# Kernel optimization log

Hardware: AMD Instinct MI355X
Metric: run time of the kernel (lower is better)

Reference implementation:

```python
import jax, jax.numpy as jnp
import numpy as np

B, L, C = 2, 2048, 256
H, HD = 8, 32          # num_heads, head_dim
BS = 16                # block_size
WS = 64                # slide_window_size
SK = 16                # select_k
SCALE = 1.0 / np.sqrt(HD)
NEG = -10000.0


def setup_inputs() -> dict:
    key = jax.random.key(0)
    ks = jax.random.split(key, 16)
    lin = lambda k, sh: jax.random.normal(k, sh, jnp.float32) * (1.0 / np.sqrt(sh[0]))
    return {
        "query": jax.random.normal(ks[0], (B, L, C), jnp.float32),
        "key": jax.random.normal(ks[1], (B, L, C), jnp.float32),
        "value": jax.random.normal(ks[2], (B, L, C), jnp.float32),
        "Wq": lin(ks[3], (C, C)), "bq": jnp.zeros((C,), jnp.float32),
        "Wk": lin(ks[4], (C, C)), "bk": jnp.zeros((C,), jnp.float32),
        "Wv": lin(ks[5], (C, C)), "bv": jnp.zeros((C,), jnp.float32),
        "Wo": lin(ks[6], (C, C)), "bo": jnp.zeros((C,), jnp.float32),
        "WKc": jax.random.normal(ks[7], (BS, 1), jnp.float32) * 0.25,
        "WVc": jax.random.normal(ks[8], (BS, 1), jnp.float32) * 0.25,
        "Wpe": jax.random.normal(ks[9], (BS, C), jnp.float32) * 0.02,
        "Wg": lin(ks[10], (C, 3)), "bg": jnp.zeros((3,), jnp.float32),
    }


def _heads(x):  # [B,T,C] -> [B,H,T,HD]
    return x.reshape(B, -1, H, HD).transpose(0, 2, 1, 3)


def _merge(x):  # [B,H,T,HD] -> [B,T,C]
    return x.transpose(0, 2, 1, 3).reshape(B, -1, C)


def _compressed(q, k, v, WKc, WVc, Wpe):
    nb = L // BS
    pe = Wpe[:, :HD]                                   # [BS,HD]
    kb = k.reshape(B, H, nb, BS, HD) + pe              # [B,H,nb,BS,HD]
    vb = v.reshape(B, H, nb, BS, HD) + pe
    Kc = jnp.einsum('bhnsd,s->bhnd', kb, WKc[:, 0])    # [B,H,nb,HD]
    Vc = jnp.einsum('bhnsd,s->bhnd', vb, WVc[:, 0])
    scores = jnp.einsum('bhqd,bhkd->bhqk', q, Kc) * SCALE
    w = jax.nn.softmax(scores, axis=-1)
    return _merge(jnp.einsum('bhqk,bhkd->bhqd', w, Vc))


def _selection(q, k, v):
    scores = jnp.einsum('bhqd,bhkd->bhqk', q, k) * SCALE   # [B,H,L,S]
    _, idx = jax.lax.top_k(scores, SK)                     # [B,H,L,SK]
    gather = lambda t: jnp.take_along_axis(t[:, :, None, :, :], idx[..., None], axis=3)
    k_sel = gather(k)                                      # [B,H,L,SK,HD]
    v_sel = gather(v)
    s = jnp.einsum('bhqd,bhqkd->bhqk', q, k_sel) * SCALE
    w = jax.nn.softmax(s, axis=-1)
    return _merge(jnp.einsum('bhqk,bhqkd->bhqd', w, v_sel))


def _window(q, k, v):
    i = jnp.arange(L)
    mask = jnp.abs(i[:, None] - i[None, :]) <= (min(WS, L) // 2)   # [L,L]
    scores = jnp.einsum('bhqd,bhkd->bhqk', q, k) * SCALE
    scores = jnp.where(mask[None, None], scores, NEG)
    w = jax.nn.softmax(scores, axis=-1)
    return _merge(jnp.einsum('bhqk,bhkd->bhqd', w, v))


def reference(query, key, value, Wq, bq, Wk, bk, Wv, bv, Wo, bo, WKc, WVc, Wpe, Wg, bg):
    q = _heads(query @ Wq + bq)
    k = _heads(key @ Wk + bk)
    v = _heads(value @ Wv + bv)
    o_cmp = _compressed(q, k, v, WKc, WVc, Wpe)
    o_slc = _selection(q, k, v)
    o_win = _window(q, k, v)
    gate = jax.nn.sigmoid(query @ Wg + bg)                 # [B,L,3]
    out = gate[:, :, 0:1] * o_cmp + gate[:, :, 1:2] * o_slc + gate[:, :, 2:3] * o_win
    return out @ Wo + bo
```

## Files before the change

kernel.cpp:

```cpp
#include <hip/hip_runtime.h>
#include <math.h>


#define Bc 2
#define Lc 2048
#define Cc 256
#define Hc 8
#define HDc 32
#define BHc 16
#define NBc 128
#define ROWSc 4096
#define TROWSc 32768
#define SCALEc 0.17677669529663687f

typedef unsigned long long u64;
typedef __attribute__((ext_vector_type(8))) short short8v;
typedef __attribute__((ext_vector_type(4))) float f32x4;


__device__ __forceinline__ float dot32q(const float* qr, const float* kr) {
  const float4* k4 = (const float4*)kr;
  float p0 = 0.f, p1 = 0.f, p2 = 0.f, p3 = 0.f;
#pragma unroll
  for (int j = 0; j < 8; j += 4) {
    float4 a = k4[j], b = k4[j + 1], c = k4[j + 2], e = k4[j + 3];
    p0 += a.x * qr[4 * j + 0] + a.y * qr[4 * j + 1] + a.z * qr[4 * j + 2] + a.w * qr[4 * j + 3];
    p1 += b.x * qr[4 * j + 4] + b.y * qr[4 * j + 5] + b.z * qr[4 * j + 6] + b.w * qr[4 * j + 7];
    p2 += c.x * qr[4 * j + 8] + c.y * qr[4 * j + 9] + c.z * qr[4 * j + 10] + c.w * qr[4 * j + 11];
    p3 += e.x * qr[4 * j + 12] + e.y * qr[4 * j + 13] + e.z * qr[4 * j + 14] + e.w * qr[4 * j + 15];
  }
  return (p0 + p1) + (p2 + p3);
}

__device__ __forceinline__ unsigned short bf16rne(float f) {
  const unsigned u = __float_as_uint(f);
  return (unsigned short)((u + 0x7fffu + ((u >> 16) & 1u)) >> 16);
}

__device__ __forceinline__ int f2o(float x) {
  const int i = __float_as_int(x);
  return i >= 0 ? i : (i ^ 0x7fffffff);
}

__global__ __launch_bounds__(256) void proj_kernel(const float* __restrict__ X,
                                                   const float* __restrict__ W,
                                                   const float* __restrict__ bias,
                                                   float* __restrict__ outp, int headlayout) {
  __shared__ float xs[8 * Cc];
  const int tid = threadIdx.x;
  const int row0 = blockIdx.x * 8;
  {
    const float4* xin = (const float4*)(X + (size_t)row0 * Cc);
    float4* xsv = (float4*)xs;
    xsv[tid] = xin[tid];
    xsv[tid + 256] = xin[tid + 256];
  }
  __syncthreads();
  const int c0 = (tid & 63) * 4;
  const int rh = tid >> 6;
  float acc[2][4];
#pragma unroll
  for (int r = 0; r < 2; ++r)
#pragma unroll
    for (int c = 0; c < 4; ++c) acc[r][c] = 0.f;

#pragma unroll 4
  for (int d4 = 0; d4 < 64; ++d4) {
    const int d = d4 * 4;
    const float4 w0 = *(const float4*)(W + (size_t)(d + 0) * Cc + c0);
    const float4 w1 = *(const float4*)(W + (size_t)(d + 1) * Cc + c0);
    const float4 w2 = *(const float4*)(W + (size_t)(d + 2) * Cc + c0);
    const float4 w3 = *(const float4*)(W + (size_t)(d + 3) * Cc + c0);
#pragma unroll
    for (int r = 0; r < 2; ++r) {
      const float4 xv = *(const float4*)(xs + (rh * 2 + r) * Cc + d);
      acc[r][0] += xv.x * w0.x + xv.y * w1.x + xv.z * w2.x + xv.w * w3.x;
      acc[r][1] += xv.x * w0.y + xv.y * w1.y + xv.z * w2.y + xv.w * w3.y;
      acc[r][2] += xv.x * w0.z + xv.y * w1.z + xv.z * w2.z + xv.w * w3.z;
      acc[r][3] += xv.x * w0.w + xv.y * w1.w + xv.z * w2.w + xv.w * w3.w;
    }
  }
  const float4 bv = *(const float4*)(bias + c0);
#pragma unroll
  for (int r = 0; r < 2; ++r) {
    const int grow = row0 + rh * 2 + r;
    const float4 o = make_float4(acc[r][0] + bv.x, acc[r][1] + bv.y,
                                 acc[r][2] + bv.z, acc[r][3] + bv.w);
    if (headlayout) {
      const int b = grow >> 11, l = grow & 2047;
      const int h = c0 >> 5, dd = c0 & 31;
      *(float4*)(outp + (((size_t)(b * Hc + h) * Lc + l) * HDc + dd)) = o;
    } else {
      *(float4*)(outp + (size_t)grow * Cc + c0) = o;
    }
  }
}

__global__ __launch_bounds__(256) void gate_kernel(const float* __restrict__ query,
                                                   const float* __restrict__ Wg,
                                                   const float* __restrict__ bg,
                                                   float* __restrict__ gatep) {
  const int row = blockIdx.x * 256 + threadIdx.x;
  const float4* x4 = (const float4*)(query + (size_t)row * Cc);
  float a0 = bg[0], a1 = bg[1], a2 = bg[2];
#pragma unroll 8
  for (int d4 = 0; d4 < 64; ++d4) {
    const float4 xv = x4[d4];
    const float* wr = Wg + d4 * 12;
    a0 += xv.x * wr[0] + xv.y * wr[3] + xv.z * wr[6] + xv.w * wr[9];
    a1 += xv.x * wr[1] + xv.y * wr[4] + xv.z * wr[7] + xv.w * wr[10];
    a2 += xv.x * wr[2] + xv.y * wr[5] + xv.z * wr[8] + xv.w * wr[11];
  }
  float* g = gatep + (size_t)row * 3;
  g[0] = 1.f / (1.f + __expf(-a0));
  g[1] = 1.f / (1.f + __expf(-a1));
  g[2] = 1.f / (1.f + __expf(-a2));
}

__global__ __launch_bounds__(256) void cmpkv_kernel(const float* __restrict__ kh,
                                                    const float* __restrict__ vh,
                                                    const float* __restrict__ WKc,
                                                    const float* __restrict__ WVc,
                                                    const float* __restrict__ Wpe,
                                                    float* __restrict__ Kcp,
                                                    float* __restrict__ Vcp) {
  const int idx = blockIdx.x * 256 + threadIdx.x;
  const int d = idx & 31, n = (idx >> 5) & 127, bh = idx >> 12;
  float pk = 0.f, pv = 0.f;
#pragma unroll
  for (int s = 0; s < 16; ++s) {
    const float pe = Wpe[s * Cc + d];
    pk += pe * WKc[s];
    pv += pe * WVc[s];
  }
  const float* kp = kh + ((size_t)bh * Lc + n * 16) * HDc + d;
  const float* vp = vh + ((size_t)bh * Lc + n * 16) * HDc + d;
  float ak = pk, av = pv;
#pragma unroll
  for (int s = 0; s < 16; ++s) {
    ak += kp[s * HDc] * WKc[s];
    av += vp[s * HDc] * WVc[s];
  }
  Kcp[idx] = ak;
  Vcp[idx] = av;
}

__global__ __launch_bounds__(512) void cmp_attn_kernel(const float* __restrict__ qh,
                                                       const float* __restrict__ Kcp,
                                                       const float* __restrict__ Vcp,
                                                       float* __restrict__ ocmp) {
  __shared__ float sc[128][65];
  __shared__ float pm[8][64];
  const int tid = threadIdx.x, lane = tid & 63;
  const int w = __builtin_amdgcn_readfirstlane(tid >> 6);
  const int bh = blockIdx.y;
  const int lrow = blockIdx.x * 64 + lane;
  const float* q = qh + ((size_t)bh * Lc + lrow) * HDc;
  float qr[HDc];
#pragma unroll
  for (int d = 0; d < HDc; ++d) qr[d] = q[d] * SCALEc;
  const float* kcb = Kcp + (size_t)bh * NBc * HDc;
  float pmax = -1e30f;
#pragma unroll
  for (int i = 0; i < 16; ++i) {
    const int key = w * 16 + i;
    const float s = dot32q(qr, kcb + (size_t)key * HDc);
    sc[key][lane] = s;
    pmax = fmaxf(pmax, s);
  }
  pm[w][lane] = pmax;
  __syncthreads();

  const int row = tid >> 3;
  const int dg = (tid & 7) * 4;
  float m = pm[0][row];
#pragma unroll
  for (int i = 1; i < 8; ++i) m = fmaxf(m, pm[i][row]);
  const float* vcb = Vcp + (size_t)bh * NBc * HDc + dg;
  float o0 = 0.f, o1 = 0.f, o2 = 0.f, o3 = 0.f, z = 0.f;
#pragma unroll 4
  for (int key = 0; key < 128; ++key) {
    const float wgt = __expf(sc[key][row] - m);
    z += wgt;
    const float4 v = *(const float4*)(vcb + key * HDc);
    o0 += wgt * v.x; o1 += wgt * v.y; o2 += wgt * v.z; o3 += wgt * v.w;
  }
  const float iz = 1.f / z;
  *(float4*)(ocmp + ((size_t)bh * Lc + blockIdx.x * 64 + row) * HDc + dg) =
      make_float4(o0 * iz, o1 * iz, o2 * iz, o3 * iz);
}

__global__ __launch_bounds__(256) void cvtbf16_kernel(const float* __restrict__ qh,
                                                      const float* __restrict__ kh,
                                                      unsigned short* __restrict__ qhb,
                                                      unsigned short* __restrict__ khb) {
  const int gid = blockIdx.x * 256 + threadIdx.x;
  const int half = (TROWSc * HDc) / 4;
  const float* src = gid < half ? qh : kh;
  unsigned short* dst = gid < half ? qhb : khb;
  const int i = (gid < half ? gid : gid - half) * 4;
  const float4 v = *(const float4*)(src + i);
  ushort4 o;
  o.x = bf16rne(v.x);
  o.y = bf16rne(v.y);
  o.z = bf16rne(v.z);
  o.w = bf16rne(v.w);
  *(ushort4*)(dst + i) = o;
}

__global__ __launch_bounds__(512) void mfma_sel_kernel(
    const unsigned short* __restrict__ qhb,
    const unsigned short* __restrict__ khb,
    const float* __restrict__ qh,
    const float* __restrict__ kh,
    const float* __restrict__ vh,
    float* __restrict__ oslc) {
  __shared__ unsigned char pnl[16][2064];
  __shared__ float candv[8][16];
  __shared__ unsigned candk[8][128];
  __shared__ u64 ords[8][128];
  const int tid = threadIdx.x, lane = tid & 63;
  const int w = __builtin_amdgcn_readfirstlane(tid >> 6);
  const int g = lane >> 4;
  const int mn = lane & 15;
  const int bh = blockIdx.y;
  const int r0 = blockIdx.x * 16;

  const short8v qa =
      *(const short8v*)(qhb + ((size_t)bh * Lc + r0 + mn) * HDc + g * 8);
#pragma unroll
  for (int it = 0; it < 2; ++it) {
    const int k0 = w * 256 + it * 128;
    const unsigned short* kbase = khb + ((size_t)bh * Lc + k0) * HDc + g * 8;
    f32x4 acc0 = {0.f, 0.f, 0.f, 0.f}, acc1 = acc0, acc2 = acc0, acc3 = acc0;
    f32x4 acc4 = acc0, acc5 = acc0, acc6 = acc0, acc7 = acc0;
#define MM(i, dstv)                                                            \
  {                                                                            \
    const short8v kb = *(const short8v*)(kbase + (size_t)((i)*16 + mn) * HDc); \
    dstv = __builtin_amdgcn_mfma_f32_16x16x32_bf16(qa, kb, dstv, 0, 0, 0);     \
  }
    MM(0, acc0) MM(1, acc1) MM(2, acc2) MM(3, acc3)
    MM(4, acc4) MM(5, acc5) MM(6, acc6) MM(7, acc7)
#undef MM
#define QSTORE(t, accv)                                                        \
  {                                                                            \
    _Pragma("unroll") for (int r = 0; r < 4; ++r) {                            \
      const float s = accv[r] * SCALEc;                                        \
      int qi = (int)(s * 16.f + 128.f);                                        \
      qi = qi < 0 ? 0 : (qi > 255 ? 255 : qi);                                 \
      pnl[4 * g + r][k0 + (t)*16 + mn] = (unsigned char)qi;                    \
    }                                                                          \
  }
    QSTORE(0, acc0) QSTORE(1, acc1) QSTORE(2, acc2) QSTORE(3, acc3)
    QSTORE(4, acc4) QSTORE(5, acc5) QSTORE(6, acc6) QSTORE(7, acc7)
#undef QSTORE
  }
  __syncthreads();

#pragma unroll 1
  for (int rr = 0; rr < 2; ++rr) {
    const int row = w * 2 + rr;
    const int l = r0 + row;
    const int r = bh * Lc + l;

    unsigned wds[8];
#pragma unroll
    for (int j = 0; j < 8; ++j)
      wds[j] = *(const unsigned*)&pnl[row][lane * 4 + j * 256];
    int q[32];
#pragma unroll
    for (int wi = 0; wi < 8; ++wi) {
      q[4 * wi + 0] = (int)(wds[wi] & 255u);
      q[4 * wi + 1] = (int)((wds[wi] >> 8) & 255u);
      q[4 * wi + 2] = (int)((wds[wi] >> 16) & 255u);
      q[4 * wi + 3] = (int)(wds[wi] >> 24);
    }
    int mq = 0;
#pragma unroll
    for (int i = 0; i < 32; ++i) mq = max(mq, q[i]);

    int T8 = 0;
#pragma unroll
    for (int b = 7; b >= 0; --b) {
      const int trial = T8 | (1 << b);
      const int c = (int)__popcll(__ballot(mq >= trial));
      if (c >= 16) T8 = trial;
    }
    const int thr = T8 - 5;

    candk[w][lane] = 0x7fffffffu;
    candk[w][64 + lane] = 0x7fffffffu;
    __asm__ volatile("s_waitcnt lgkmcnt(0)" ::: "memory");
    int base = 0;
#pragma unroll
    for (int i = 0; i < 32; ++i) {
      const bool p_ = q[i] >= thr;
      const unsigned long long bm_ = __ballot(p_);
      if (bm_) {
        if (p_) {
          const int pos_ =
              base + (int)__builtin_amdgcn_mbcnt_hi(
                         (unsigned)(bm_ >> 32),
                         __builtin_amdgcn_mbcnt_lo((unsigned)bm_, 0u));
          if (pos_ < 128)
            candk[w][pos_] = (unsigned)((i >> 2) * 256 + lane * 4 + (i & 3));
        }
        base += (int)__popcll(bm_);
      }
    }
    const int cnt = base < 128 ? base : 128;
    __asm__ volatile("s_waitcnt lgkmcnt(0)" ::: "memory");

    const float* qp = qh + (size_t)r * HDc;
    float qr[HDc];
#pragma unroll
    for (int d = 0; d < HDc; ++d) qr[d] = qp[d] * SCALEc;
    const float* kb = kh + (size_t)bh * Lc * HDc;

    const bool vA = (lane < cnt);
    const bool vB = (64 + lane < cnt);
    const unsigned kA = candk[w][lane];
    const unsigned kB = candk[w][64 + lane];
    const float sA = dot32q(qr, kb + (size_t)(vA ? kA : 0u) * HDc);
    const float sB = dot32q(qr, kb + (size_t)(vB ? kB : 0u) * HDc);
    const u64 ordA =
        vA ? (((u64)((unsigned)f2o(sA) ^ 0x80000000u) << 12) | (u64)(2047u - kA))
           : 0ull;
    const u64 ordB =
        vB ? (((u64)((unsigned)f2o(sB) ^ 0x80000000u) << 12) | (u64)(2047u - kB))
           : 0ull;

    ords[w][lane] = ordA;
    ords[w][64 + lane] = ordB;
    __asm__ volatile("s_waitcnt lgkmcnt(0)" ::: "memory");
    int rankA = 0, rankB = 0;
#pragma unroll 4
    for (int i = 0; i < cnt; ++i) {
      const u64 o = ords[w][i];
      rankA += (o > ordA) ? 1 : 0;
      rankB += (o > ordB) ? 1 : 0;
    }
    if (vA && rankA < 16) {
      candv[w][rankA] = sA;
      candk[w][rankA] = kA;
    }
    if (vB && rankB < 16) {
      candv[w][rankB] = sB;
      candk[w][rankB] = kB;
    }
    __asm__ volatile("s_waitcnt lgkmcnt(0)" ::: "memory");

    float mtop = candv[w][0];
#pragma unroll
    for (int i = 1; i < 16; ++i) mtop = fmaxf(mtop, candv[w][i]);
    const int d = lane & 31;
    const float* vb = vh + (size_t)bh * Lc * HDc + d;
    float z = 0.f, oacc = 0.f;
#pragma unroll
    for (int i = 0; i < 16; ++i) {
      const float w_ = __expf(candv[w][i] - mtop);
      z += w_;
      oacc += w_ * vb[(size_t)candk[w][i] * HDc];
    }
    if (lane < 32) oslc[((size_t)bh * Lc + l) * HDc + d] = oacc / z;
  }
}

__global__ __launch_bounds__(512) void win_attn_kernel(const float* __restrict__ qh,
                                                       const float* __restrict__ kh,
                                                       const float* __restrict__ vh,
                                                       float* __restrict__ owin) {
  __shared__ float sc[128][65];
  __shared__ float pm[8][64];
  const int tid = threadIdx.x, lane = tid & 63;
  const int w = __builtin_amdgcn_readfirstlane(tid >> 6);
  const int bh = blockIdx.y;
  const int l0 = blockIdx.x * 64;
  const int lrow = l0 + lane;
  const float* q = qh + ((size_t)bh * Lc + lrow) * HDc;
  float qr[HDc];
#pragma unroll
  for (int d = 0; d < HDc; ++d) qr[d] = q[d] * SCALEc;
  const float* kb = kh + (size_t)bh * Lc * HDc;
  float pmax = -1e30f;
#pragma unroll
  for (int i = 0; i < 16; ++i) {
    const int j = w * 16 + i;
    const int key = l0 - 32 + j;
    const int keyc = min(max(key, 0), Lc - 1);
    float s = dot32q(qr, kb + (size_t)keyc * HDc);
    const int delta = key - lrow;
    const bool ok = (key >= 0) && (key < Lc) && (delta >= -32) && (delta <= 32);
    s = ok ? s : -1e30f;
    sc[j][lane] = s;
    pmax = fmaxf(pmax, s);
  }
  pm[w][lane] = pmax;
  __syncthreads();

  const int row = tid >> 3;
  const int dg = (tid & 7) * 4;
  float m = pm[0][row];
#pragma unroll
  for (int i = 1; i < 8; ++i) m = fmaxf(m, pm[i][row]);
  const float* vb = vh + (size_t)bh * Lc * HDc + dg;
  float o0 = 0.f, o1 = 0.f, o2 = 0.f, o3 = 0.f, z = 0.f;
#pragma unroll 4
  for (int j = 0; j < 128; ++j) {
    const float wgt = __expf(sc[j][row] - m);
    z += wgt;
    const int keyc = min(max(l0 - 32 + j, 0), Lc - 1);
    const float4 v = *(const float4*)(vb + (size_t)keyc * HDc);
    o0 += wgt * v.x; o1 += wgt * v.y; o2 += wgt * v.z; o3 += wgt * v.w;
  }
  const float iz = 1.f / z;
  *(float4*)(owin + ((size_t)bh * Lc + l0 + row) * HDc + dg) =
      make_float4(o0 * iz, o1 * iz, o2 * iz, o3 * iz);
}

__global__ __launch_bounds__(256) void combine_kernel(const float* __restrict__ ocmp,
                                                      const float* __restrict__ oslc,
                                                      const float* __restrict__ owin,
                                                      const float* __restrict__ gatep,
                                                      float* __restrict__ xm) {
  const int idx = blockIdx.x * 256 + threadIdx.x;
  const int c4 = idx & 63, grow = idx >> 6;
  const int b = grow >> 11, l = grow & 2047;
  const int h = c4 >> 3, d4 = (c4 & 7) * 4;
  const size_t hoff = (((size_t)(b * Hc + h) * Lc + l)) * HDc + d4;
  const float g0 = gatep[(size_t)grow * 3 + 0];
  const float g1 = gatep[(size_t)grow * 3 + 1];
  const float g2 = gatep[(size_t)grow * 3 + 2];
  const float4 a = *(const float4*)(ocmp + hoff);
  const float4 s = *(const float4*)(oslc + hoff);
  const float4 w = *(const float4*)(owin + hoff);
  float4 r;
  r.x = g0 * a.x + g1 * s.x + g2 * w.x;
  r.y = g0 * a.y + g1 * s.y + g2 * w.y;
  r.z = g0 * a.z + g1 * s.z + g2 * w.z;
  r.w = g0 * a.w + g1 * s.w + g2 * w.w;
  *(float4*)(xm + (size_t)grow * Cc + c4 * 4) = r;
}

extern "C" void kernel_launch(void* const* d_in, const int* in_sizes, int n_in,
                              void* d_out, int out_size, void* d_ws, size_t ws_size,
                              hipStream_t stream) {
  (void)in_sizes; (void)n_in; (void)out_size; (void)ws_size;
  const float* query = (const float*)d_in[0];
  const float* key   = (const float*)d_in[1];
  const float* value = (const float*)d_in[2];
  const float* Wq = (const float*)d_in[3];
  const float* bq = (const float*)d_in[4];
  const float* Wk = (const float*)d_in[5];
  const float* bk = (const float*)d_in[6];
  const float* Wv = (const float*)d_in[7];
  const float* bv = (const float*)d_in[8];
  const float* Wo = (const float*)d_in[9];
  const float* bo = (const float*)d_in[10];
  const float* WKc = (const float*)d_in[11];
  const float* WVc = (const float*)d_in[12];
  const float* Wpe = (const float*)d_in[13];
  const float* Wg = (const float*)d_in[14];
  const float* bg = (const float*)d_in[15];

  size_t off = 0;
  auto alloc = [&](size_t bytes) -> void* {
    void* p = (char*)d_ws + off;
    off += (bytes + 255) & ~(size_t)255;
    return p;
  };
  float* qh    = (float*)alloc((size_t)TROWSc * HDc * 4);
  float* kh    = (float*)alloc((size_t)TROWSc * HDc * 4);
  float* vh    = (float*)alloc((size_t)TROWSc * HDc * 4);
  float* gatep = (float*)alloc((size_t)ROWSc * 3 * 4);
  float* Kcp   = (float*)alloc((size_t)BHc * NBc * HDc * 4);
  float* Vcp   = (float*)alloc((size_t)BHc * NBc * HDc * 4);
  float* ocmp  = (float*)alloc((size_t)TROWSc * HDc * 4);
  float* oslc  = (float*)alloc((size_t)TROWSc * HDc * 4);
  float* owin  = (float*)alloc((size_t)TROWSc * HDc * 4);
  float* xm    = (float*)alloc((size_t)ROWSc * Cc * 4);
  unsigned short* qhb = (unsigned short*)alloc((size_t)TROWSc * HDc * 2);
  unsigned short* khb = (unsigned short*)alloc((size_t)TROWSc * HDc * 2);

  proj_kernel<<<dim3(512), 256, 0, stream>>>(query, Wq, bq, qh, 1);
  proj_kernel<<<dim3(512), 256, 0, stream>>>(key, Wk, bk, kh, 1);
  proj_kernel<<<dim3(512), 256, 0, stream>>>(value, Wv, bv, vh, 1);
  gate_kernel<<<dim3(16), 256, 0, stream>>>(query, Wg, bg, gatep);
  cmpkv_kernel<<<dim3(256), 256, 0, stream>>>(kh, vh, WKc, WVc, Wpe, Kcp, Vcp);
  cmp_attn_kernel<<<dim3(32, 16), 512, 0, stream>>>(qh, Kcp, Vcp, ocmp);
  cvtbf16_kernel<<<dim3(2048), 256, 0, stream>>>(qh, kh, qhb, khb);
  mfma_sel_kernel<<<dim3(128, 16), 512, 0, stream>>>(qhb, khb, qh, kh, vh, oslc);
  win_attn_kernel<<<dim3(32, 16), 512, 0, stream>>>(qh, kh, vh, owin);
  combine_kernel<<<dim3(1024), 256, 0, stream>>>(ocmp, oslc, owin, gatep, xm);
  proj_kernel<<<dim3(512), 256, 0, stream>>>(xm, Wo, bo, (float*)d_out, 0);
}
```

Baseline: 242.9 us.

## Fuse bf16 conversion into projection and widen selection kernel to 1024 threads

The Q and K projection kernels now also write bf16 copies of their outputs, so the separate conversion kernel and its extra read of the fp32 head tensors are removed. The selection kernel now runs 16 waves per block, one query row and 128 keys per wave, instead of 8 waves each handling two rows and 256 keys. This adds parallelism per block, but 1024-thread blocks with larger shared arrays may lower occupancy or raise register pressure.

```diff
diff --git a/kernel.cpp b/kernel.cpp
--- a/kernel.cpp
+++ b/kernel.cpp
@@ -45,7 +45,9 @@
 __global__ __launch_bounds__(256) void proj_kernel(const float* __restrict__ X,
                                                    const float* __restrict__ W,
                                                    const float* __restrict__ bias,
-                                                   float* __restrict__ outp, int headlayout) {
+                                                   float* __restrict__ outp,
+                                                   unsigned short* __restrict__ outb,
+                                                   int headlayout) {
   __shared__ float xs[8 * Cc];
   const int tid = threadIdx.x;
   const int row0 = blockIdx.x * 8;
@@ -89,7 +91,16 @@
     if (headlayout) {
       const int b = grow >> 11, l = grow & 2047;
       const int h = c0 >> 5, dd = c0 & 31;
-      *(float4*)(outp + (((size_t)(b * Hc + h) * Lc + l) * HDc + dd)) = o;
+      const size_t hoff = ((size_t)(b * Hc + h) * Lc + l) * HDc + dd;
+      *(float4*)(outp + hoff) = o;
+      if (outb) {
+        ushort4 ob;
+        ob.x = bf16rne(o.x);
+        ob.y = bf16rne(o.y);
+        ob.z = bf16rne(o.z);
+        ob.w = bf16rne(o.w);
+        *(ushort4*)(outb + hoff) = ob;
+      }
     } else {
       *(float4*)(outp + (size_t)grow * Cc + c0) = o;
     }
@@ -190,25 +201,7 @@
       make_float4(o0 * iz, o1 * iz, o2 * iz, o3 * iz);
 }
 
-__global__ __launch_bounds__(256) void cvtbf16_kernel(const float* __restrict__ qh,
-                                                      const float* __restrict__ kh,
-                                                      unsigned short* __restrict__ qhb,
-                                                      unsigned short* __restrict__ khb) {
-  const int gid = blockIdx.x * 256 + threadIdx.x;
-  const int half = (TROWSc * HDc) / 4;
-  const float* src = gid < half ? qh : kh;
-  unsigned short* dst = gid < half ? qhb : khb;
-  const int i = (gid < half ? gid : gid - half) * 4;
-  const float4 v = *(const float4*)(src + i);
-  ushort4 o;
-  o.x = bf16rne(v.x);
-  o.y = bf16rne(v.y);
-  o.z = bf16rne(v.z);
-  o.w = bf16rne(v.w);
-  *(ushort4*)(dst + i) = o;
-}
-
-__global__ __launch_bounds__(512) void mfma_sel_kernel(
+__global__ __launch_bounds__(1024) void mfma_sel_kernel(
     const unsigned short* __restrict__ qhb,
     const unsigned short* __restrict__ khb,
     const float* __restrict__ qh,
@@ -216,9 +209,9 @@
     const float* __restrict__ vh,
     float* __restrict__ oslc) {
   __shared__ unsigned char pnl[16][2064];
-  __shared__ float candv[8][16];
-  __shared__ unsigned candk[8][128];
-  __shared__ u64 ords[8][128];
+  __shared__ float candv[16][16];
+  __shared__ unsigned candk[16][128];
+  __shared__ u64 ords[16][128];
   const int tid = threadIdx.x, lane = tid & 63;
   const int w = __builtin_amdgcn_readfirstlane(tid >> 6);
   const int g = lane >> 4;
@@ -228,9 +221,8 @@
 
   const short8v qa =
       *(const short8v*)(qhb + ((size_t)bh * Lc + r0 + mn) * HDc + g * 8);
-#pragma unroll
-  for (int it = 0; it < 2; ++it) {
-    const int k0 = w * 256 + it * 128;
+  {
+    const int k0 = w * 128;
     const unsigned short* kbase = khb + ((size_t)bh * Lc + k0) * HDc + g * 8;
     f32x4 acc0 = {0.f, 0.f, 0.f, 0.f}, acc1 = acc0, acc2 = acc0, acc3 = acc0;
     f32x4 acc4 = acc0, acc5 = acc0, acc6 = acc0, acc7 = acc0;
@@ -257,9 +249,8 @@
   }
   __syncthreads();
 
-#pragma unroll 1
-  for (int rr = 0; rr < 2; ++rr) {
-    const int row = w * 2 + rr;
+  {
+    const int row = w;
     const int l = r0 + row;
     const int r = bh * Lc + l;
 
@@ -482,15 +473,14 @@
   unsigned short* qhb = (unsigned short*)alloc((size_t)TROWSc * HDc * 2);
   unsigned short* khb = (unsigned short*)alloc((size_t)TROWSc * HDc * 2);
 
-  proj_kernel<<<dim3(512), 256, 0, stream>>>(query, Wq, bq, qh, 1);
-  proj_kernel<<<dim3(512), 256, 0, stream>>>(key, Wk, bk, kh, 1);
-  proj_kernel<<<dim3(512), 256, 0, stream>>>(value, Wv, bv, vh, 1);
+  proj_kernel<<<dim3(512), 256, 0, stream>>>(query, Wq, bq, qh, qhb, 1);
+  proj_kernel<<<dim3(512), 256, 0, stream>>>(key, Wk, bk, kh, khb, 1);
+  proj_kernel<<<dim3(512), 256, 0, stream>>>(value, Wv, bv, vh, (unsigned short*)0, 1);
   gate_kernel<<<dim3(16), 256, 0, stream>>>(query, Wg, bg, gatep);
   cmpkv_kernel<<<dim3(256), 256, 0, stream>>>(kh, vh, WKc, WVc, Wpe, Kcp, Vcp);
   cmp_attn_kernel<<<dim3(32, 16), 512, 0, stream>>>(qh, Kcp, Vcp, ocmp);
-  cvtbf16_kernel<<<dim3(2048), 256, 0, stream>>>(qh, kh, qhb, khb);
-  mfma_sel_kernel<<<dim3(128, 16), 512, 0, stream>>>(qhb, khb, qh, kh, vh, oslc);
+  mfma_sel_kernel<<<dim3(128, 16), 1024, 0, stream>>>(qhb, khb, qh, kh, vh, oslc);
   win_attn_kernel<<<dim3(32, 16), 512, 0, stream>>>(qh, kh, vh, owin);
   combine_kernel<<<dim3(1024), 256, 0, stream>>>(ocmp, oslc, owin, gatep, xm);
-  proj_kernel<<<dim3(512), 256, 0, stream>>>(xm, Wo, bo, (float*)d_out, 0);
-}
+  proj_kernel<<<dim3(512), 256, 0, stream>>>(xm, Wo, bo, (float*)d_out, (unsigned short*)0, 0);
+}
```

Measured after the change: 286.0 us. 1.18x slower.

## Merge compressed, selection and window attention into one interleaved launch

Applied to the files above, without the earlier changes.

The three separate attention kernels are combined into a single launch of 3072 blocks. Each group of six blocks holds four selection tiles, one compressed tile and one window tile, and all three share one shared-memory buffer. This removes two launch gaps and lets the light compressed and window work run alongside the heavier selection blocks. The cost is that every block reserves the largest shared-memory footprint, which can lower occupancy for the smaller bodies, and register allocation is now set by the heaviest branch.

```diff
diff --git a/kernel.cpp b/kernel.cpp
--- a/kernel.cpp
+++ b/kernel.cpp
@@ -143,51 +143,6 @@
   }
   Kcp[idx] = ak;
   Vcp[idx] = av;
-}
-
-__global__ __launch_bounds__(512) void cmp_attn_kernel(const float* __restrict__ qh,
-                                                       const float* __restrict__ Kcp,
-                                                       const float* __restrict__ Vcp,
-                                                       float* __restrict__ ocmp) {
-  __shared__ float sc[128][65];
-  __shared__ float pm[8][64];
-  const int tid = threadIdx.x, lane = tid & 63;
-  const int w = __builtin_amdgcn_readfirstlane(tid >> 6);
-  const int bh = blockIdx.y;
-  const int lrow = blockIdx.x * 64 + lane;
-  const float* q = qh + ((size_t)bh * Lc + lrow) * HDc;
-  float qr[HDc];
-#pragma unroll
-  for (int d = 0; d < HDc; ++d) qr[d] = q[d] * SCALEc;
-  const float* kcb = Kcp + (size_t)bh * NBc * HDc;
-  float pmax = -1e30f;
-#pragma unroll
-  for (int i = 0; i < 16; ++i) {
-    const int key = w * 16 + i;
-    const float s = dot32q(qr, kcb + (size_t)key * HDc);
-    sc[key][lane] = s;
-    pmax = fmaxf(pmax, s);
-  }
-  pm[w][lane] = pmax;
-  __syncthreads();
-
-  const int row = tid >> 3;
-  const int dg = (tid & 7) * 4;
-  float m = pm[0][row];
-#pragma unroll
-  for (int i = 1; i < 8; ++i) m = fmaxf(m, pm[i][row]);
-  const float* vcb = Vcp + (size_t)bh * NBc * HDc + dg;
-  float o0 = 0.f, o1 = 0.f, o2 = 0.f, o3 = 0.f, z = 0.f;
-#pragma unroll 4
-  for (int key = 0; key < 128; ++key) {
-    const float wgt = __expf(sc[key][row] - m);
-    z += wgt;
-    const float4 v = *(const float4*)(vcb + key * HDc);
-    o0 += wgt * v.x; o1 += wgt * v.y; o2 += wgt * v.z; o3 += wgt * v.w;
-  }
-  const float iz = 1.f / z;
-  *(float4*)(ocmp + ((size_t)bh * Lc + blockIdx.x * 64 + row) * HDc + dg) =
-      make_float4(o0 * iz, o1 * iz, o2 * iz, o3 * iz);
 }
 
 __global__ __launch_bounds__(256) void cvtbf16_kernel(const float* __restrict__ qh,
@@ -208,23 +163,121 @@
   *(ushort4*)(dst + i) = o;
 }
 
-__global__ __launch_bounds__(512) void mfma_sel_kernel(
-    const unsigned short* __restrict__ qhb,
-    const unsigned short* __restrict__ khb,
-    const float* __restrict__ qh,
-    const float* __restrict__ kh,
-    const float* __restrict__ vh,
-    float* __restrict__ oslc) {
-  __shared__ unsigned char pnl[16][2064];
-  __shared__ float candv[8][16];
-  __shared__ unsigned candk[8][128];
-  __shared__ u64 ords[8][128];
+#define SMEM_BYTES 45824
+
+__device__ void cmp_attn_body(unsigned char* smraw, int bx, int bh,
+                              const float* __restrict__ qh,
+                              const float* __restrict__ Kcp,
+                              const float* __restrict__ Vcp,
+                              float* __restrict__ ocmp) {
+  float (*sc)[65] = (float(*)[65])smraw;
+  float (*pm)[64] = (float(*)[64])(smraw + 33280);
+  const int tid = threadIdx.x, lane = tid & 63;
+  const int w = __builtin_amdgcn_readfirstlane(tid >> 6);
+  const int lrow = bx * 64 + lane;
+  const float* q = qh + ((size_t)bh * Lc + lrow) * HDc;
+  float qr[HDc];
+#pragma unroll
+  for (int d = 0; d < HDc; ++d) qr[d] = q[d] * SCALEc;
+  const float* kcb = Kcp + (size_t)bh * NBc * HDc;
+  float pmax = -1e30f;
+#pragma unroll
+  for (int i = 0; i < 16; ++i) {
+    const int key = w * 16 + i;
+    const float s = dot32q(qr, kcb + (size_t)key * HDc);
+    sc[key][lane] = s;
+    pmax = fmaxf(pmax, s);
+  }
+  pm[w][lane] = pmax;
+  __syncthreads();
+
+  const int row = tid >> 3;
+  const int dg = (tid & 7) * 4;
+  float m = pm[0][row];
+#pragma unroll
+  for (int i = 1; i < 8; ++i) m = fmaxf(m, pm[i][row]);
+  const float* vcb = Vcp + (size_t)bh * NBc * HDc + dg;
+  float o0 = 0.f, o1 = 0.f, o2 = 0.f, o3 = 0.f, z = 0.f;
+#pragma unroll 4
+  for (int key = 0; key < 128; ++key) {
+    const float wgt = __expf(sc[key][row] - m);
+    z += wgt;
+    const float4 v = *(const float4*)(vcb + key * HDc);
+    o0 += wgt * v.x; o1 += wgt * v.y; o2 += wgt * v.z; o3 += wgt * v.w;
+  }
+  const float iz = 1.f / z;
+  *(float4*)(ocmp + ((size_t)bh * Lc + bx * 64 + row) * HDc + dg) =
+      make_float4(o0 * iz, o1 * iz, o2 * iz, o3 * iz);
+}
+
+__device__ void win_attn_body(unsigned char* smraw, int bx, int bh,
+                              const float* __restrict__ qh,
+                              const float* __restrict__ kh,
+                              const float* __restrict__ vh,
+                              float* __restrict__ owin) {
+  float (*sc)[65] = (float(*)[65])smraw;
+  float (*pm)[64] = (float(*)[64])(smraw + 33280);
+  const int tid = threadIdx.x, lane = tid & 63;
+  const int w = __builtin_amdgcn_readfirstlane(tid >> 6);
+  const int l0 = bx * 64;
+  const int lrow = l0 + lane;
+  const float* q = qh + ((size_t)bh * Lc + lrow) * HDc;
+  float qr[HDc];
+#pragma unroll
+  for (int d = 0; d < HDc; ++d) qr[d] = q[d] * SCALEc;
+  const float* kb = kh + (size_t)bh * Lc * HDc;
+  float pmax = -1e30f;
+#pragma unroll
+  for (int i = 0; i < 16; ++i) {
+    const int j = w * 16 + i;
+    const int key = l0 - 32 + j;
+    const int keyc = min(max(key, 0), Lc - 1);
+    float s = dot32q(qr, kb + (size_t)keyc * HDc);
+    const int delta = key - lrow;
+    const bool ok = (key >= 0) && (key < Lc) && (delta >= -32) && (delta <= 32);
+    s = ok ? s : -1e30f;
+    sc[j][lane] = s;
+    pmax = fmaxf(pmax, s);
+  }
+  pm[w][lane] = pmax;
+  __syncthreads();
+
+  const int row = tid >> 3;
+  const int dg = (tid & 7) * 4;
+  float m = pm[0][row];
+#pragma unroll
+  for (int i = 1; i < 8; ++i) m = fmaxf(m, pm[i][row]);
+  const float* vb = vh + (size_t)bh * Lc * HDc + dg;
+  float o0 = 0.f, o1 = 0.f, o2 = 0.f, o3 = 0.f, z = 0.f;
+#pragma unroll 4
+  for (int j = 0; j < 128; ++j) {
+    const float wgt = __expf(sc[j][row] - m);
+    z += wgt;
+    const int keyc = min(max(l0 - 32 + j, 0), Lc - 1);
+    const float4 v = *(const float4*)(vb + (size_t)keyc * HDc);
+    o0 += wgt * v.x; o1 += wgt * v.y; o2 += wgt * v.z; o3 += wgt * v.w;
+  }
+  const float iz = 1.f / z;
+  *(float4*)(owin + ((size_t)bh * Lc + l0 + row) * HDc + dg) =
+      make_float4(o0 * iz, o1 * iz, o2 * iz, o3 * iz);
+}
+
+__device__ void sel_body(unsigned char* smraw, int rowtile, int bh,
+                         const unsigned short* __restrict__ qhb,
+                         const unsigned short* __restrict__ khb,
+                         const float* __restrict__ qh,
+                         const float* __restrict__ kh,
+                         const float* __restrict__ vh,
+                         float* __restrict__ oslc) {
+  unsigned char (*pnl)[2064] = (unsigned char(*)[2064])smraw;
+  float (*candv)[16] = (float(*)[16])(smraw + 33024);
+  unsigned (*candk)[128] = (unsigned(*)[128])(smraw + 33536);
+  u64 (*ords)[128] = (u64(*)[128])(smraw + 37632);
   const int tid = threadIdx.x, lane = tid & 63;
   const int w = __builtin_amdgcn_readfirstlane(tid >> 6);
   const int g = lane >> 4;
   const int mn = lane & 15;
-  const int bh = blockIdx.y;
-  const int r0 = blockIdx.x * 16;
+  const int r0 = rowtile * 16;
 
   const short8v qa =
       *(const short8v*)(qhb + ((size_t)bh * Lc + r0 + mn) * HDc + g * 8);
@@ -366,56 +419,28 @@
   }
 }
 
-__global__ __launch_bounds__(512) void win_attn_kernel(const float* __restrict__ qh,
-                                                       const float* __restrict__ kh,
-                                                       const float* __restrict__ vh,
-                                                       float* __restrict__ owin) {
-  __shared__ float sc[128][65];
-  __shared__ float pm[8][64];
-  const int tid = threadIdx.x, lane = tid & 63;
-  const int w = __builtin_amdgcn_readfirstlane(tid >> 6);
-  const int bh = blockIdx.y;
-  const int l0 = blockIdx.x * 64;
-  const int lrow = l0 + lane;
-  const float* q = qh + ((size_t)bh * Lc + lrow) * HDc;
-  float qr[HDc];
-#pragma unroll
-  for (int d = 0; d < HDc; ++d) qr[d] = q[d] * SCALEc;
-  const float* kb = kh + (size_t)bh * Lc * HDc;
-  float pmax = -1e30f;
-#pragma unroll
-  for (int i = 0; i < 16; ++i) {
-    const int j = w * 16 + i;
-    const int key = l0 - 32 + j;
-    const int keyc = min(max(key, 0), Lc - 1);
-    float s = dot32q(qr, kb + (size_t)keyc * HDc);
-    const int delta = key - lrow;
-    const bool ok = (key >= 0) && (key < Lc) && (delta >= -32) && (delta <= 32);
-    s = ok ? s : -1e30f;
-    sc[j][lane] = s;
-    pmax = fmaxf(pmax, s);
-  }
-  pm[w][lane] = pmax;
-  __syncthreads();
-
-  const int row = tid >> 3;
-  const int dg = (tid & 7) * 4;
-  float m = pm[0][row];
-#pragma unroll
-  for (int i = 1; i < 8; ++i) m = fmaxf(m, pm[i][row]);
-  const float* vb = vh + (size_t)bh * Lc * HDc + dg;
-  float o0 = 0.f, o1 = 0.f, o2 = 0.f, o3 = 0.f, z = 0.f;
-#pragma unroll 4
-  for (int j = 0; j < 128; ++j) {
-    const float wgt = __expf(sc[j][row] - m);
-    z += wgt;
-    const int keyc = min(max(l0 - 32 + j, 0), Lc - 1);
-    const float4 v = *(const float4*)(vb + (size_t)keyc * HDc);
-    o0 += wgt * v.x; o1 += wgt * v.y; o2 += wgt * v.z; o3 += wgt * v.w;
-  }
-  const float iz = 1.f / z;
-  *(float4*)(owin + ((size_t)bh * Lc + l0 + row) * HDc + dg) =
-      make_float4(o0 * iz, o1 * iz, o2 * iz, o3 * iz);
+__global__ __launch_bounds__(512) void attn_fused_kernel(
+    const unsigned short* __restrict__ qhb,
+    const unsigned short* __restrict__ khb,
+    const float* __restrict__ qh,
+    const float* __restrict__ kh,
+    const float* __restrict__ vh,
+    const float* __restrict__ Kcp,
+    const float* __restrict__ Vcp,
+    float* __restrict__ ocmp,
+    float* __restrict__ oslc,
+    float* __restrict__ owin) {
+  __shared__ __align__(16) unsigned char smraw[SMEM_BYTES];
+  const int bid = blockIdx.x;
+  const int grp = bid / 6, rpos = bid % 6;
+  if (rpos < 4) {
+    const int idx = grp * 4 + rpos;
+    sel_body(smraw, idx & 127, idx >> 7, qhb, khb, qh, kh, vh, oslc);
+  } else if (rpos == 4) {
+    cmp_attn_body(smraw, grp & 31, grp >> 5, qh, Kcp, Vcp, ocmp);
+  } else {
+    win_attn_body(smraw, grp & 31, grp >> 5, qh, kh, vh, owin);
+  }
 }
 
 __global__ __launch_bounds__(256) void combine_kernel(const float* __restrict__ ocmp,
@@ -487,10 +512,9 @@
   proj_kernel<<<dim3(512), 256, 0, stream>>>(value, Wv, bv, vh, 1);
   gate_kernel<<<dim3(16), 256, 0, stream>>>(query, Wg, bg, gatep);
   cmpkv_kernel<<<dim3(256), 256, 0, stream>>>(kh, vh, WKc, WVc, Wpe, Kcp, Vcp);
-  cmp_attn_kernel<<<dim3(32, 16), 512, 0, stream>>>(qh, Kcp, Vcp, ocmp);
   cvtbf16_kernel<<<dim3(2048), 256, 0, stream>>>(qh, kh, qhb, khb);
-  mfma_sel_kernel<<<dim3(128, 16), 512, 0, stream>>>(qhb, khb, qh, kh, vh, oslc);
-  win_attn_kernel<<<dim3(32, 16), 512, 0, stream>>>(qh, kh, vh, owin);
+  attn_fused_kernel<<<dim3(3072), 512, 0, stream>>>(qhb, khb, qh, kh, vh, Kcp,
+                                                    Vcp, ocmp, oslc, owin);
   combine_kernel<<<dim3(1024), 256, 0, stream>>>(ocmp, oslc, owin, gatep, xm);
   proj_kernel<<<dim3(512), 256, 0, stream>>>(xm, Wo, bo, (float*)d_out, 0);
 }
```

Result: no change. 242.1 us (-0.4%).
